# Optimization experiments

Measured on AMD Instinct MI355X. Metric: run time of the kernel, lower is better.

Reference implementation:

```python
import jax, jax.numpy as jnp
import numpy as np

N_HEAD, N_KV_HEAD, HEAD_DIM = 16, 4, 128
EPS = 1e-5


def rms_norm(x, eps=EPS):
    return x * jax.lax.rsqrt(jnp.mean(x * x, axis=-1, keepdims=True) + eps)


def apply_rope(x, cos, sin):
    # x: (B,T,H,D); cos/sin: (1,T,1,D//2)
    d = x.shape[-1] // 2
    x1, x2 = x[..., :d], x[..., d:]
    return jnp.concatenate([x1 * cos - x2 * sin, x1 * sin + x2 * cos], axis=-1)


def setup_inputs() -> dict:
    key = jax.random.key(0)
    ks = jax.random.split(key, 6)
    B, T, C = 4, 2048, 2048
    H, KV, D = N_HEAD, N_KV_HEAD, HEAD_DIM
    x = jax.random.normal(ks[0], (B, T, C), dtype=jnp.float32)
    # RoPE tables (llama-style, theta=10000)
    inv_freq = 1.0 / (10000.0 ** (jnp.arange(D // 2, dtype=jnp.float32) / (D // 2)))
    ang = jnp.arange(T, dtype=jnp.float32)[:, None] * inv_freq[None, :]  # (T, D/2)
    cos = jnp.cos(ang)[None, :, None, :]
    sin = jnp.sin(ang)[None, :, None, :]
    s = 0.02
    wq = jax.random.normal(ks[1], (C, H * D), dtype=jnp.float32) * s
    wk = jax.random.normal(ks[2], (C, KV * D), dtype=jnp.float32) * s
    wv = jax.random.normal(ks[3], (C, KV * D), dtype=jnp.float32) * s
    wproj = jax.random.normal(ks[4], (H * D, C), dtype=jnp.float32) * s
    return {"x": x, "cos": cos, "sin": sin, "wq": wq, "wk": wk, "wv": wv, "wproj": wproj}


def reference(x, cos, sin, wq, wk, wv, wproj):
    B, T, C = x.shape
    H, KV, D = N_HEAD, N_KV_HEAD, HEAD_DIM
    n_rep = H // KV
    q = (x @ wq).reshape(B, T, H, D)
    k = (x @ wk).reshape(B, T, KV, D)
    v = (x @ wv).reshape(B, T, KV, D)
    q = apply_rope(q, cos, sin)
    k = apply_rope(k, cos, sin)
    # QK-norm (use_qk_norm=True)
    q = rms_norm(q)
    k = rms_norm(k)
    # GQA: expand kv heads (matches torch repeat_interleave on head dim)
    k = jnp.repeat(k, n_rep, axis=2)
    v = jnp.repeat(v, n_rep, axis=2)
    scale = 1.0 / np.sqrt(D).astype(np.float32)
    scores = jnp.einsum('bqhd,bkhd->bhqk', q, k) * scale  # (B,H,T,T)
    causal = jnp.tril(jnp.ones((T, T), dtype=bool))
    scores = jnp.where(causal[None, None], scores, jnp.finfo(scores.dtype).min)
    p = jax.nn.softmax(scores, axis=-1)
    y = jnp.einsum('bhqk,bkhd->bqhd', p, v).reshape(B, T, H * D)
    return y @ wproj
```

## Files before the change

kernel.cpp:

```cpp
#include <hip/hip_runtime.h>
#include <hip/hip_bf16.h>
#include <stdint.h>

using bf16 = __hip_bfloat16;
typedef __attribute__((ext_vector_type(8))) short short8;
typedef __attribute__((ext_vector_type(4))) float f32x4;
typedef __attribute__((ext_vector_type(16))) float f32x16;

#define MFMA16(a,b,c) __builtin_amdgcn_mfma_f32_16x16x32_bf16(a,b,c,0,0,0)
#define MFMA32(a,b,c) __builtin_amdgcn_mfma_f32_32x32x16_bf16(a,b,c,0,0,0)

__device__ __forceinline__ void gload_lds16(const void* g, void* l) {
  __builtin_amdgcn_global_load_lds((const __attribute__((address_space(1))) void*)g,
                                   (__attribute__((address_space(3))) void*)l, 16, 0, 0);
}

__device__ __forceinline__ short bf_bits(float f) {
  bf16 h = __float2bfloat16(f);
  return *reinterpret_cast<short*>(&h);
}
__device__ __forceinline__ unsigned int pk2(float a, float b) {
  return ((unsigned int)(unsigned short)bf_bits(b) << 16) | (unsigned short)bf_bits(a);
}

__global__ __launch_bounds__(256) void f32_to_bf16_k(const float* __restrict__ in,
                                                     bf16* __restrict__ out, size_t n) {
  size_t i = ((size_t)blockIdx.x * 256 + threadIdx.x) * 8;
  if (i >= n) return;
  float4 a = *(const float4*)(in + i);
  float4 b = *(const float4*)(in + i + 4);
  short8 pk;
  pk[0] = bf_bits(a.x); pk[1] = bf_bits(a.y); pk[2] = bf_bits(a.z); pk[3] = bf_bits(a.w);
  pk[4] = bf_bits(b.x); pk[5] = bf_bits(b.y); pk[6] = bf_bits(b.z); pk[7] = bf_bits(b.w);
  *(short8*)(out + i) = pk;
}

__global__ __launch_bounds__(256) void transpose_cvt_k(const float* __restrict__ in,
                                                       bf16* __restrict__ out, int K, int N) {
  __shared__ float tile[32][33];
  int n0 = blockIdx.x * 32, k0 = blockIdx.y * 32;
  int tx = threadIdx.x & 31, ty = threadIdx.x >> 5;
#pragma unroll
  for (int j = 0; j < 4; ++j) {
    int kk = ty + j * 8;
    tile[kk][tx] = in[(size_t)(k0 + kk) * N + n0 + tx];
  }
  __syncthreads();
#pragma unroll
  for (int j = 0; j < 4; ++j) {
    int nn = ty + j * 8;
    out[(size_t)(n0 + nn) * K + k0 + tx] = __float2bfloat16(tile[tx][nn]);
  }
}

__global__ __launch_bounds__(256) void transpose_v_k(const bf16* __restrict__ qkv,
                                                     bf16* __restrict__ vt) {
  constexpr int T = 2048, Dh = 128, KV = 4, QKVW = 3072, VOFF = 2560;
  __shared__ bf16 tile[32][33];
  int t0 = blockIdx.x * 32, d0 = blockIdx.y * 32;
  int b = blockIdx.z >> 2, kv = blockIdx.z & 3;
  int tx = threadIdx.x & 31, ty = threadIdx.x >> 5;
#pragma unroll
  for (int j = 0; j < 4; ++j) {
    int tt = ty + j * 8;
    tile[tt][tx] = qkv[((size_t)(b * T + t0 + tt)) * QKVW + VOFF + kv * Dh + d0 + tx];
  }
  __syncthreads();
#pragma unroll
  for (int j = 0; j < 4; ++j) {
    int dd = ty + j * 8;
    vt[((size_t)((b * KV + kv) * Dh + d0 + dd)) * T + t0 + tx] = tile[tx][dd];
  }
}

__global__ __launch_bounds__(256) void rope_rms_k(bf16* __restrict__ buf, int rowstride,
                                                  int baseoff,
                                                  const float* __restrict__ cosp,
                                                  const float* __restrict__ sinp,
                                                  int nh, float outscale) {
  constexpr int T = 2048;
  int wid = blockIdx.x * 4 + (threadIdx.x >> 6);
  int lane = threadIdx.x & 63;
  int h = wid % nh;
  int tok = wid / nh;
  int t = tok & (T - 1);
  bf16* p = buf + (size_t)tok * rowstride + baseoff + h * 128;
  float x1 = __bfloat162float(p[lane]);
  float x2 = __bfloat162float(p[lane + 64]);
  float c = cosp[t * 64 + lane], s = sinp[t * 64 + lane];
  float o1 = x1 * c - x2 * s;
  float o2 = x1 * s + x2 * c;
  float ss = o1 * o1 + o2 * o2;
#pragma unroll
  for (int m = 1; m < 64; m <<= 1) ss += __shfl_xor(ss, m, 64);
  float r = rsqrtf(ss * (1.f / 128.f) + 1e-5f) * outscale;
  p[lane] = __float2bfloat16(o1 * r);
  p[lane + 64] = __float2bfloat16(o2 * r);
}

#define PHASE(buf, i0, ...)                                                       \
  {                                                                               \
    short8 a00 = ldA(buf, i0, 0), a01 = ldA(buf, i0, 1);                          \
    short8 a10 = ldA(buf, (i0) + 1, 0), a11 = ldA(buf, (i0) + 1, 1);              \
    __VA_ARGS__;                                                                  \
    __builtin_amdgcn_s_barrier();                                                 \
    asm volatile("s_waitcnt lgkmcnt(0)" ::: "memory");                            \
    __builtin_amdgcn_s_setprio(1);                                                \
    _Pragma("unroll") for (int j = 0; j < 4; ++j) {                               \
      acc[i0][j] = MFMA16(a00, bf_[2 * j], acc[i0][j]);                           \
      acc[i0][j] = MFMA16(a01, bf_[2 * j + 1], acc[i0][j]);                       \
      acc[(i0) + 1][j] = MFMA16(a10, bf_[2 * j], acc[(i0) + 1][j]);               \
      acc[(i0) + 1][j] = MFMA16(a11, bf_[2 * j + 1], acc[(i0) + 1][j]);           \
    }                                                                             \
    __builtin_amdgcn_s_setprio(0);                                                \
  }
#define LOADB(buf)                                                                \
  _Pragma("unroll") for (int j = 0; j < 4; ++j) {                                 \
    bf_[2 * j] = ldB(buf, j, 0);                                                  \
    bf_[2 * j + 1] = ldB(buf, j, 1);                                              \
  }
#define BAR __builtin_amdgcn_s_barrier()

template <typename OutT>
__global__ __launch_bounds__(512, 2) void gemm256(const bf16* __restrict__ A,
                                                  const bf16* __restrict__ Bt,
                                                  OutT* __restrict__ C, int M, int N, int K,
                                                  int NT) {
  __shared__ char lds[131072];
  const int tid = threadIdx.x, lane = tid & 63, w = tid >> 6;
  const int wm = w >> 2, wn = w & 3;
  const int bx = blockIdx.x;
  const int chunk = gridDim.x >> 3;
  const int wgid = (bx & 7) * chunk + (bx >> 3);
  const int m0 = (wgid / NT) * 256, n0 = (wgid % NT) * 256;
  const int lm = lane & 15;
  const int sw = (lane & 7) << 4;
  const int g16 = (lane >> 4) << 4;
  const size_t strideAB = (size_t)K * 2;

  auto stageA = [&](int buf, int h, int t) {
#pragma unroll
    for (int p2 = 0; p2 < 2; ++p2) {
      int off = tid * 16 + p2 * 8192;
      int row = off >> 7, cb = off & 127;
      int scb = cb ^ ((row & 7) << 4);
      gload_lds16((const char*)A + (size_t)(m0 + h * 128 + row) * strideAB + t * 128 + scb,
                  lds + buf * 65536 + h * 16384 + off);
    }
  };
  auto stageB = [&](int buf, int h, int t) {
#pragma unroll
    for (int p2 = 0; p2 < 2; ++p2) {
      int off = tid * 16 + p2 * 8192;
      int row = off >> 7, cb = off & 127;
      int scb = cb ^ ((row & 7) << 4);
      gload_lds16((const char*)Bt + (size_t)(n0 + h * 128 + row) * strideAB + t * 128 + scb,
                  lds + buf * 65536 + 32768 + h * 16384 + off);
    }
  };
  auto ldA = [&](int buf, int i, int ks) {
    int row = wm * 128 + i * 16 + lm;
    return *(const short8*)(lds + buf * 65536 + row * 128 + ((ks * 64 + g16) ^ sw));
  };
  auto ldB = [&](int buf, int j, int ks) {
    int row = wn * 64 + j * 16 + lm;
    return *(const short8*)(lds + buf * 65536 + 32768 + row * 128 + ((ks * 64 + g16) ^ sw));
  };

  f32x4 acc[8][4] = {};
  short8 bf_[8];
  const int niter = K / 128;

  stageA(0, 0, 0); stageA(0, 1, 0); stageB(0, 0, 0); stageB(0, 1, 0);
  stageB(1, 0, 1); stageB(1, 1, 1);
  asm volatile("s_waitcnt vmcnt(4)" ::: "memory");
  BAR;

  for (int i = 0; i < niter; ++i) {
    const int t0 = 2 * i, t1 = 2 * i + 1;
    const bool nl = (i + 1 < niter);
    LOADB(0);
    PHASE(0, 0, stageA(1, 0, t1)); BAR;
    PHASE(0, 2, stageA(1, 1, t1)); BAR;
    PHASE(0, 4, if (nl) stageB(0, 0, t0 + 2)); BAR;
    PHASE(0, 6, if (nl) stageB(0, 1, t0 + 2));
    if (nl) { asm volatile("s_waitcnt vmcnt(4)" ::: "memory"); }
    else    { asm volatile("s_waitcnt vmcnt(0)" ::: "memory"); }
    BAR;
    LOADB(1);
    PHASE(1, 0, if (nl) stageA(0, 0, t0 + 2)); BAR;
    PHASE(1, 2, if (nl) stageA(0, 1, t0 + 2)); BAR;
    PHASE(1, 4, if (nl) stageB(1, 0, t1 + 2)); BAR;
    PHASE(1, 6, if (nl) stageB(1, 1, t1 + 2));
    if (nl) { asm volatile("s_waitcnt vmcnt(4)" ::: "memory"); }
    BAR;
  }

  if constexpr (sizeof(OutT) == 2) {
    __syncthreads();
    bf16* sC = (bf16*)lds;
#pragma unroll
    for (int i = 0; i < 8; ++i) {
      int row = wm * 128 + i * 16 + (lane >> 4) * 4;
#pragma unroll
      for (int j = 0; j < 4; ++j) {
        int col = wn * 64 + j * 16 + lm;
#pragma unroll
        for (int r = 0; r < 4; ++r) sC[(row + r) * 256 + col] = __float2bfloat16(acc[i][j][r]);
      }
    }
    __syncthreads();
#pragma unroll
    for (int p = 0; p < 16; ++p) {
      int off = tid * 16 + p * 8192;
      int row = off >> 9, cb = off & 511;
      *(short8*)((char*)C + ((size_t)(m0 + row) * N + n0) * 2 + cb) =
          *(const short8*)(lds + off);
    }
  } else {
#pragma unroll
    for (int i = 0; i < 8; ++i) {
      int row = m0 + wm * 128 + i * 16 + (lane >> 4) * 4;
#pragma unroll
      for (int j = 0; j < 4; ++j) {
        int col = n0 + wn * 64 + j * 16 + lm;
#pragma unroll
        for (int r = 0; r < 4; ++r) C[(size_t)(row + r) * N + col] = acc[i][j][r];
      }
    }
  }
}

__global__ __launch_bounds__(512, 2) void attn_k(const bf16* __restrict__ qkv,
                                                 const bf16* __restrict__ vt,
                                                 bf16* __restrict__ y) {
  constexpr int T = 2048, Dh = 128, KV = 4, KB = 64, QKVW = 3072, KOFF = 2048;
  __shared__ char lds[65536];
  const int tid = threadIdx.x, lane = tid & 63, w = tid >> 6;
  const int hi = lane >> 5, lq = lane & 31;
  const int bx = blockIdx.x;
  const int qt = 7 - (bx >> 6);
  const int b = (bx >> 4) & 3, h = bx & 15;
  const int kh = h >> 2;
  const int q0 = qt * 256 + w * 32;
  const int qg = q0 + lq;
  const int swz = (lane & 7) << 4;

  short8 aq[8];
  {
    const bf16* qp = qkv + ((size_t)(b * T + qg)) * QKVW + h * Dh + hi * 8;
#pragma unroll
    for (int m = 0; m < 8; ++m) aq[m] = *(const short8*)(qp + m * 16);
  }
  __builtin_amdgcn_s_waitcnt(0);

  f32x16 acc[4] = {};
  float mrow = -1e4f, lrow = 0.f;

  auto stage = [&](int buf, int kv0) {
#pragma unroll
    for (int p = 0; p < 2; ++p) {
      int off = tid * 16 + p * 8192;
      int row = off >> 8, cb = off & 255;
      int scb = cb ^ ((row & 7) << 4);
      gload_lds16((const char*)qkv + (((size_t)(b * T + kv0 + row)) * QKVW + KOFF + kh * Dh) * 2 + scb,
                  lds + buf * 16384 + off);
    }
#pragma unroll
    for (int p = 0; p < 2; ++p) {
      int off = tid * 16 + p * 8192;
      int row = off >> 7, cb = off & 127;
      int scb = cb ^ ((row & 7) << 4);
      gload_lds16((const char*)vt + (((size_t)((b * KV + kh) * Dh + row)) * T + kv0) * 2 + scb,
                  lds + 32768 + buf * 16384 + off);
    }
  };

  const int nt = (qt + 1) * 4;
  const int lastit = (q0 + 31) >> 6;
  stage(0, 0);

  for (int it = 0; it < nt; ++it) {
    int cur = it & 1;
    if (it + 1 < nt) { stage(cur ^ 1, (it + 1) * KB); asm volatile("s_waitcnt vmcnt(4)" ::: "memory"); }
    else             { asm volatile("s_waitcnt vmcnt(0)" ::: "memory"); }
    __builtin_amdgcn_s_barrier();
    if (it <= lastit) {
      const char* sK = lds + cur * 16384;
      const char* sV = lds + 32768 + cur * 16384;
      const int kv0 = it * KB;

      f32x16 s0 = {}, s1 = {};
      __builtin_amdgcn_s_setprio(1);
#pragma unroll
      for (int m = 0; m < 8; ++m) {
        short8 ak = *(const short8*)(sK + lq * 256 + ((m * 32 + hi * 16) ^ swz));
        s0 = MFMA32(ak, aq[m], s0);
      }
#pragma unroll
      for (int m = 0; m < 8; ++m) {
        short8 ak = *(const short8*)(sK + (32 + lq) * 256 + ((m * 32 + hi * 16) ^ swz));
        s1 = MFMA32(ak, aq[m], s1);
      }
      __builtin_amdgcn_s_setprio(0);

      if (kv0 + 63 > q0) {
#pragma unroll
        for (int r = 0; r < 16; ++r) {
          int krow = (r & 3) + 8 * (r >> 2) + 4 * hi;
          if (kv0 + krow > qg) s0[r] = -1e30f;
          if (kv0 + 32 + krow > qg) s1[r] = -1e30f;
        }
      }

      float tmax = s0[0];
#pragma unroll
      for (int r = 1; r < 16; ++r) tmax = fmaxf(tmax, s0[r]);
#pragma unroll
      for (int r = 0; r < 16; ++r) tmax = fmaxf(tmax, s1[r]);
      tmax = fmaxf(tmax, __shfl_xor(tmax, 32, 64));
      if (!__all(tmax - mrow <= 8.0f)) {
        float mn = fmaxf(mrow, tmax);
        float corr = __expf(mrow - mn);
        mrow = mn;
        lrow *= corr;
#pragma unroll
        for (int dt = 0; dt < 4; ++dt)
#pragma unroll
          for (int r = 0; r < 16; ++r) acc[dt][r] *= corr;
      }
      float rsum = 0.f;
#pragma unroll
      for (int r = 0; r < 16; ++r) { s0[r] = __expf(s0[r] - mrow); rsum += s0[r]; }
#pragma unroll
      for (int r = 0; r < 16; ++r) { s1[r] = __expf(s1[r] - mrow); rsum += s1[r]; }
      rsum += __shfl_xor(rsum, 32, 64);
      lrow += rsum;

      unsigned int u[16];
#pragma unroll
      for (int g = 0; g < 4; ++g) {
        u[g * 2 + 0] = pk2(s0[4 * g + 0], s0[4 * g + 1]);
        u[g * 2 + 1] = pk2(s0[4 * g + 2], s0[4 * g + 3]);
        u[8 + g * 2 + 0] = pk2(s1[4 * g + 0], s1[4 * g + 1]);
        u[8 + g * 2 + 1] = pk2(s1[4 * g + 2], s1[4 * g + 3]);
      }
      short8 pb[4];
#pragma unroll
      for (int kvs = 0; kvs < 4; ++kvs) {
        unsigned int lo0 = u[4 * kvs + 0], lo1 = u[4 * kvs + 1];
        unsigned int hi0 = u[4 * kvs + 2], hi1 = u[4 * kvs + 3];
        asm volatile("v_permlane32_swap_b32 %0, %1" : "+v"(lo0), "+v"(hi0));
        asm volatile("v_permlane32_swap_b32 %0, %1" : "+v"(lo1), "+v"(hi1));
        union { short8 v; unsigned int q[4]; } P;
        P.q[0] = lo0; P.q[1] = lo1; P.q[2] = hi0; P.q[3] = hi1;
        pb[kvs] = P.v;
      }

      __builtin_amdgcn_s_setprio(1);
#pragma unroll
      for (int dt = 0; dt < 4; ++dt) {
#pragma unroll
        for (int kvs = 0; kvs < 4; ++kvs) {
          short8 av = *(const short8*)(sV + (dt * 32 + lq) * 128 + ((kvs * 32 + hi * 16) ^ swz));
          acc[dt] = MFMA32(av, pb[kvs], acc[dt]);
        }
      }
      __builtin_amdgcn_s_setprio(0);
    }
    __builtin_amdgcn_s_barrier();
  }

  float inv = 1.f / lrow;
  __syncthreads();
  char* myO = lds + w * 8192;
#pragma unroll
  for (int dt = 0; dt < 4; ++dt)
#pragma unroll
    for (int i = 0; i < 8; ++i) {
      int d = ((2 * i) & 3) + 8 * (i >> 1) + 4 * hi;
      unsigned int pkd = pk2(acc[dt][2 * i] * inv, acc[dt][2 * i + 1] * inv);
      *(unsigned int*)(myO + lq * 256 + ((dt * 64 + d * 2) ^ ((lq & 7) << 4))) = pkd;
    }
  __syncthreads();
  const int row0 = b * T + qt * 256;
#pragma unroll
  for (int p = 0; p < 8; ++p) {
    int off = (p * 512 + tid) * 16;
    int q = off >> 8, cb = off & 255;
    short8 v = *(const short8*)(lds + (q >> 5) * 8192 + (q & 31) * 256 + (cb ^ ((q & 7) << 4)));
    *(short8*)((char*)y + ((size_t)(row0 + q) * 2048 + h * 128) * 2 + cb) = v;
  }
}

extern "C" void kernel_launch(void* const* d_in, const int* in_sizes, int n_in,
                              void* d_out, int out_size, void* d_ws, size_t ws_size,
                              hipStream_t stream) {
  const float* x    = (const float*)d_in[0];
  const float* cosp = (const float*)d_in[1];
  const float* sinp = (const float*)d_in[2];
  const float* wq   = (const float*)d_in[3];
  const float* wk   = (const float*)d_in[4];
  const float* wv   = (const float*)d_in[5];
  const float* wp   = (const float*)d_in[6];
  float* out = (float*)d_out;

  constexpr size_t Mtok = 8192;
  constexpr int Cdim = 2048, HD = 2048, KVD = 512, QKVW = 3072;

  char* ws = (char*)d_ws;
  bf16* xb    = (bf16*)ws; ws += Mtok * Cdim * 2;
  bf16* wqkvT = (bf16*)ws; ws += (size_t)QKVW * Cdim * 2;
  bf16* wpT   = (bf16*)ws; ws += (size_t)Cdim * HD * 2;
  bf16* qkv   = (bf16*)ws; ws += Mtok * QKVW * 2;
  bf16* vtb   = (bf16*)ws; ws += Mtok * KVD * 2;
  bf16* yb    = (bf16*)ws; ws += Mtok * HD * 2;

  f32_to_bf16_k<<<dim3(Mtok * Cdim / 8 / 256), 256, 0, stream>>>(x, xb, Mtok * Cdim);
  transpose_cvt_k<<<dim3(HD / 32, Cdim / 32), 256, 0, stream>>>(wq, wqkvT, Cdim, HD);
  transpose_cvt_k<<<dim3(KVD / 32, Cdim / 32), 256, 0, stream>>>(wk, wqkvT + (size_t)2048 * Cdim, Cdim, KVD);
  transpose_cvt_k<<<dim3(KVD / 32, Cdim / 32), 256, 0, stream>>>(wv, wqkvT + (size_t)2560 * Cdim, Cdim, KVD);
  transpose_cvt_k<<<dim3(Cdim / 32, HD / 32), 256, 0, stream>>>(wp, wpT, HD, Cdim);

  gemm256<bf16><<<dim3(384), 512, 0, stream>>>(xb, wqkvT, qkv, (int)Mtok, QKVW, Cdim, 12);

  rope_rms_k<<<dim3(Mtok * 16 / 4), 256, 0, stream>>>(qkv, QKVW, 0, cosp, sinp, 16,
                                                      0.08838834764831845f);
  rope_rms_k<<<dim3(Mtok * 4 / 4), 256, 0, stream>>>(qkv, QKVW, 2048, cosp, sinp, 4, 1.0f);
  transpose_v_k<<<dim3(64, 4, 16), 256, 0, stream>>>(qkv, vtb);

  attn_k<<<dim3(512), 512, 0, stream>>>(qkv, vtb, yb);

  gemm256<float><<<dim3(256), 512, 0, stream>>>(yb, wpT, out, (int)Mtok, HD, Cdim, 8);
}
```

Baseline: 342.3 us.

## Fuse Q RoPE and RMS norm into attention; split QKV GEMM into Q and KV parts

The Q-head RoPE and RMS norm pass is removed and done inside the attention kernel on the Q fragments held in registers, reading cos/sin directly. This drops one full read and write of the Q section of the qkv buffer. The QKV projection is also split: the Q part (N=2048) uses the 256x256 gemm, and the K/V part (N=1024) uses a new simpler 128x128 single-buffered gemm. The new gemm has no swizzle and no double buffering, which may leave the smaller K/V projection slower. Q is rounded to bf16 before normalisation, which slightly changes numerics.

```diff
diff --git a/kernel.cpp b/kernel.cpp
--- a/kernel.cpp
+++ b/kernel.cpp
@@ -21,6 +21,9 @@
 }
 __device__ __forceinline__ unsigned int pk2(float a, float b) {
   return ((unsigned int)(unsigned short)bf_bits(b) << 16) | (unsigned short)bf_bits(a);
+}
+__device__ __forceinline__ float bf2f(short s) {
+  return __uint_as_float((unsigned int)(unsigned short)s << 16);
 }
 
 __global__ __launch_bounds__(256) void f32_to_bf16_k(const float* __restrict__ in,
@@ -124,8 +127,8 @@
 template <typename OutT>
 __global__ __launch_bounds__(512, 2) void gemm256(const bf16* __restrict__ A,
                                                   const bf16* __restrict__ Bt,
-                                                  OutT* __restrict__ C, int M, int N, int K,
-                                                  int NT) {
+                                                  OutT* __restrict__ C, int K,
+                                                  int NT, int ldC) {
   __shared__ char lds[131072];
   const int tid = threadIdx.x, lane = tid & 63, w = tid >> 6;
   const int wm = w >> 2, wn = w & 3;
@@ -214,7 +217,7 @@
     for (int p = 0; p < 16; ++p) {
       int off = tid * 16 + p * 8192;
       int row = off >> 9, cb = off & 511;
-      *(short8*)((char*)C + ((size_t)(m0 + row) * N + n0) * 2 + cb) =
+      *(short8*)((char*)C + ((size_t)(m0 + row) * ldC + n0) * 2 + cb) =
           *(const short8*)(lds + off);
     }
   } else {
@@ -225,7 +228,93 @@
       for (int j = 0; j < 4; ++j) {
         int col = n0 + wn * 64 + j * 16 + lm;
 #pragma unroll
-        for (int r = 0; r < 4; ++r) C[(size_t)(row + r) * N + col] = acc[i][j][r];
+        for (int r = 0; r < 4; ++r) C[(size_t)(row + r) * ldC + col] = acc[i][j][r];
+      }
+    }
+  }
+}
+
+template <typename OutT>
+__global__ __launch_bounds__(256) void gemm_bt(const bf16* __restrict__ A,
+                                               const bf16* __restrict__ Bt,
+                                               OutT* __restrict__ C, int K,
+                                               int NT, int ldC) {
+  constexpr int BM = 128, BN = 128, BK = 64;
+  __shared__ char smem[32768];
+  bf16* sA = (bf16*)smem;
+  bf16* sB = (bf16*)(smem + 16384);
+  int tid = threadIdx.x;
+  int lane = tid & 63, w = tid >> 6;
+  int flat = blockIdx.x;
+  int wgid = (flat & 7) * (gridDim.x >> 3) + (flat >> 3);
+  int m0 = (wgid / NT) * BM, n0 = (wgid % NT) * BN;
+  int wm = (w >> 1) * 64, wn = (w & 1) * 64;
+  f32x4 acc[4][4] = {};
+  int nk = K / BK;
+  for (int kt = 0; kt < nk; ++kt) {
+    __syncthreads();
+    int kb = kt * BK;
+#pragma unroll
+    for (int it = 0; it < 4; ++it) {
+      int off = tid * 16 + it * 4096;
+      int row = off >> 7, cb = off & 127;
+      gload_lds16((const char*)A + (((size_t)(m0 + row)) * K + kb) * 2 + cb, (char*)sA + off);
+    }
+#pragma unroll
+    for (int it = 0; it < 4; ++it) {
+      int off = tid * 16 + it * 4096;
+      int row = off >> 7, cb = off & 127;
+      gload_lds16((const char*)Bt + (((size_t)(n0 + row)) * K + kb) * 2 + cb, (char*)sB + off);
+    }
+    asm volatile("s_waitcnt vmcnt(0)" ::: "memory");
+    __syncthreads();
+#pragma unroll
+    for (int ks = 0; ks < 2; ++ks) {
+      short8 af[4], bfr[4];
+#pragma unroll
+      for (int i = 0; i < 4; ++i) {
+        af[i]  = *(const short8*)(sA + (wm + i * 16 + (lane & 15)) * BK + ks * 32 + (lane >> 4) * 8);
+        bfr[i] = *(const short8*)(sB + (wn + i * 16 + (lane & 15)) * BK + ks * 32 + (lane >> 4) * 8);
+      }
+#pragma unroll
+      for (int i = 0; i < 4; ++i)
+#pragma unroll
+        for (int j = 0; j < 4; ++j)
+          acc[i][j] = MFMA16(af[i], bfr[j], acc[i][j]);
+    }
+  }
+  if constexpr (sizeof(OutT) == 2) {
+    __syncthreads();
+    bf16* sC = (bf16*)smem;
+#pragma unroll
+    for (int i = 0; i < 4; ++i) {
+      int row = wm + i * 16 + (lane >> 4) * 4;
+#pragma unroll
+      for (int j = 0; j < 4; ++j) {
+        int col = wn + j * 16 + (lane & 15);
+#pragma unroll
+        for (int r = 0; r < 4; ++r)
+          sC[(row + r) * BN + col] = __float2bfloat16(acc[i][j][r]);
+      }
+    }
+    __syncthreads();
+#pragma unroll
+    for (int it = 0; it < 8; ++it) {
+      int off = tid * 16 + it * 4096;
+      int row = off >> 8, cb = off & 255;
+      *(short8*)((char*)C + ((size_t)(m0 + row) * ldC + n0) * 2 + cb) =
+          *(const short8*)(smem + off);
+    }
+  } else {
+#pragma unroll
+    for (int i = 0; i < 4; ++i) {
+      int row = m0 + wm + i * 16 + (lane >> 4) * 4;
+#pragma unroll
+      for (int j = 0; j < 4; ++j) {
+        int col = n0 + wn + j * 16 + (lane & 15);
+#pragma unroll
+        for (int r = 0; r < 4; ++r)
+          C[(size_t)(row + r) * ldC + col] = acc[i][j][r];
       }
     }
   }
@@ -233,7 +322,9 @@
 
 __global__ __launch_bounds__(512, 2) void attn_k(const bf16* __restrict__ qkv,
                                                  const bf16* __restrict__ vt,
-                                                 bf16* __restrict__ y) {
+                                                 bf16* __restrict__ y,
+                                                 const float* __restrict__ cosp,
+                                                 const float* __restrict__ sinp) {
   constexpr int T = 2048, Dh = 128, KV = 4, KB = 64, QKVW = 3072, KOFF = 2048;
   __shared__ char lds[65536];
   const int tid = threadIdx.x, lane = tid & 63, w = tid >> 6;
@@ -254,6 +345,33 @@
   }
   __builtin_amdgcn_s_waitcnt(0);
 
+  {
+    float ss = 0.f;
+#pragma unroll
+    for (int m = 0; m < 8; ++m)
+#pragma unroll
+      for (int e = 0; e < 8; ++e) { float v = bf2f(aq[m][e]); ss += v * v; }
+    ss += __shfl_xor(ss, 32, 64);
+    float rn = rsqrtf(ss * (1.f / 128.f) + 1e-5f) * 0.08838834764831845f;
+    const float4* cq4 = (const float4*)(cosp + (size_t)qg * 64) + hi * 2;
+    const float4* sq4 = (const float4*)(sinp + (size_t)qg * 64) + hi * 2;
+#pragma unroll
+    for (int m = 0; m < 4; ++m) {
+      float4 c0 = cq4[m * 4], c1 = cq4[m * 4 + 1];
+      float4 s0 = sq4[m * 4], s1 = sq4[m * 4 + 1];
+      float cc[8] = {c0.x, c0.y, c0.z, c0.w, c1.x, c1.y, c1.z, c1.w};
+      float sn[8] = {s0.x, s0.y, s0.z, s0.w, s1.x, s1.y, s1.z, s1.w};
+      short8 xl = aq[m], xh = aq[m + 4], nl, nh;
+#pragma unroll
+      for (int e = 0; e < 8; ++e) {
+        float x1 = bf2f(xl[e]), x2 = bf2f(xh[e]);
+        nl[e] = bf_bits((x1 * cc[e] - x2 * sn[e]) * rn);
+        nh[e] = bf_bits((x1 * sn[e] + x2 * cc[e]) * rn);
+      }
+      aq[m] = nl; aq[m + 4] = nh;
+    }
+  }
+
   f32x16 acc[4] = {};
   float mrow = -1e4f, lrow = 0.f;
 
@@ -422,14 +540,14 @@
   transpose_cvt_k<<<dim3(KVD / 32, Cdim / 32), 256, 0, stream>>>(wv, wqkvT + (size_t)2560 * Cdim, Cdim, KVD);
   transpose_cvt_k<<<dim3(Cdim / 32, HD / 32), 256, 0, stream>>>(wp, wpT, HD, Cdim);
 
-  gemm256<bf16><<<dim3(384), 512, 0, stream>>>(xb, wqkvT, qkv, (int)Mtok, QKVW, Cdim, 12);
-
-  rope_rms_k<<<dim3(Mtok * 16 / 4), 256, 0, stream>>>(qkv, QKVW, 0, cosp, sinp, 16,
-                                                      0.08838834764831845f);
+  gemm256<bf16><<<dim3(256), 512, 0, stream>>>(xb, wqkvT, qkv, Cdim, 8, QKVW);
+  gemm_bt<bf16><<<dim3(512), 256, 0, stream>>>(xb, wqkvT + (size_t)2048 * Cdim,
+                                               (bf16*)qkv + 2048, Cdim, 8, QKVW);
+
   rope_rms_k<<<dim3(Mtok * 4 / 4), 256, 0, stream>>>(qkv, QKVW, 2048, cosp, sinp, 4, 1.0f);
   transpose_v_k<<<dim3(64, 4, 16), 256, 0, stream>>>(qkv, vtb);
 
-  attn_k<<<dim3(512), 512, 0, stream>>>(qkv, vtb, yb);
-
-  gemm256<float><<<dim3(256), 512, 0, stream>>>(yb, wpT, out, (int)Mtok, HD, Cdim, 8);
-}
+  attn_k<<<dim3(512), 512, 0, stream>>>(qkv, vtb, yb, cosp, sinp);
+
+  gemm256<float><<<dim3(256), 512, 0, stream>>>(yb, wpT, out, Cdim, 8, 2048);
+}
```

Result: faster. 322.6 us (-5.7%).
